# Performance work log

Measured on AMD Instinct MI355X. Metric: run time of the kernel, lower is better.

## Reference

```python
import jax, jax.numpy as jnp
import numpy as np

B, T, C = 2, 1024, 2048
HEAD_SIZE = 64
H = C // HEAD_SIZE          # 32 heads
N_LAYER, LAYER_ID = 24, 12
D_MIX_LORA = 32
LN_EPS = 1e-5


def _layer_norm(x, g, b):
    mu = jnp.mean(x, axis=-1, keepdims=True)
    var = jnp.mean(jnp.square(x - mu), axis=-1, keepdims=True)
    return (x - mu) * jax.lax.rsqrt(var + LN_EPS) * g + b


def setup_inputs() -> dict:
    key = jax.random.key(0)
    ks = jax.random.split(key, 8)
    # data-dependent init of time_maa_* exactly as in the torch module
    r01 = LAYER_ID / (N_LAYER - 1)
    r1a0 = 1.0 - LAYER_ID / N_LAYER
    ddd = np.arange(C, dtype=np.float32) / C
    time_maa_x = jnp.asarray(1.0 - np.power(ddd, r1a0), dtype=jnp.float32)
    time_maa_r = jnp.asarray(1.0 - np.power(ddd, 0.5 * r1a0), dtype=jnp.float32)
    time_maa_k = jnp.asarray(1.0 - np.power(ddd, r1a0), dtype=jnp.float32)
    time_maa_v = jnp.asarray(1.0 - (np.power(ddd, r1a0) + 0.3 * r01), dtype=jnp.float32)
    # LoRA mix weights (w1 is zero-init in the module, keep small random for a nontrivial test)
    w1 = jax.random.uniform(ks[0], (C, D_MIX_LORA * 3), jnp.float32, -0.01, 0.01)
    w2 = jax.random.uniform(ks[1], (3, D_MIX_LORA, C), jnp.float32, -0.01, 0.01)
    scale = 1.0 / np.sqrt(C)
    Wq = jax.random.normal(ks[2], (C, C), jnp.float32) * scale  # stored as [in, out]
    Wk = jax.random.normal(ks[3], (C, C), jnp.float32) * scale
    Wv = jax.random.normal(ks[4], (C, C), jnp.float32) * scale
    Wo = jax.random.normal(ks[5], (C, C), jnp.float32) * scale
    ones = jnp.ones((C,), jnp.float32)
    zeros = jnp.zeros((C,), jnp.float32)
    # rotary angles, standard half-dim frequencies over head_size
    Kd = HEAD_SIZE
    inv_freq = 1.0 / (10000.0 ** (np.arange(0, Kd, 2, dtype=np.float32) / Kd))
    ang = np.outer(np.arange(T, dtype=np.float32), inv_freq)  # [T, Kd//2]
    cos = jnp.asarray(np.cos(ang), jnp.float32)
    sin = jnp.asarray(np.sin(ang), jnp.float32)
    x = jax.random.normal(ks[6], (B, T, C), jnp.float32)
    shift_state = jax.random.normal(ks[7], (B, C), jnp.float32)
    return {
        "x": x, "shift_state": shift_state,
        "time_maa_x": time_maa_x, "time_maa_r": time_maa_r,
        "time_maa_k": time_maa_k, "time_maa_v": time_maa_v,
        "w1": w1, "w2": w2,
        "Wq": Wq, "Wk": Wk, "Wv": Wv, "Wo": Wo,
        "g_r": ones, "b_r": zeros, "g_k": ones, "b_k": zeros,
        "g_v": ones, "b_v": zeros, "g_x": ones, "b_x": zeros,
        "cos": cos, "sin": sin,
    }


def reference(x, shift_state, time_maa_x, time_maa_r, time_maa_k, time_maa_v,
              w1, w2, Wq, Wk, Wv, Wo,
              g_r, b_r, g_k, b_k, g_v, b_v, g_x, b_x, cos, sin):
    Bv, Tv, Cv = x.shape
    Kd = Cv // H
    # token shift: prepend previous-step state, diff against current
    xprev = jnp.concatenate([shift_state[:, None, :], x[:, :-1]], axis=1)
    dxprev = xprev - x
    # data-dependent LoRA mixing coefficients
    xxx = x + dxprev * time_maa_x                      # [B,T,C]
    h = jnp.tanh(xxx @ w1).reshape(Bv, Tv, 3, D_MIX_LORA)
    m = jnp.einsum('btli,lic->lbtc', h, w2)            # [3,B,T,C]
    mr, mk, mv = m[0], m[1], m[2]
    xq = x + dxprev * (time_maa_r + mr)
    xk = x + dxprev * (time_maa_k + mk)
    xv = x + dxprev * (time_maa_v + mv)
    q = _layer_norm(xq @ Wq, g_r, b_r)
    k = _layer_norm(xk @ Wk, g_k, b_k)
    v = _layer_norm(xv @ Wv, g_v, b_v)
    # [B,H,T,K]
    q = q.reshape(Bv, Tv, H, Kd).transpose(0, 2, 1, 3)
    k = k.reshape(Bv, Tv, H, Kd).transpose(0, 2, 1, 3)
    v = v.reshape(Bv, Tv, H, Kd).transpose(0, 2, 1, 3)
    # rotary embedding (half split)
    c = cos[None, None, :, :]
    s = sin[None, None, :, :]
    def rope(t):
        t1, t2 = t[..., :Kd // 2], t[..., Kd // 2:]
        return jnp.concatenate([t1 * c - t2 * s, t1 * s + t2 * c], axis=-1)
    q, k = rope(q), rope(k)
    # causal SDPA
    scores = jnp.einsum('bhtd,bhsd->bhts', q, k) / np.sqrt(Kd)
    mask = jnp.tril(jnp.ones((Tv, Tv), dtype=bool))
    scores = jnp.where(mask, scores, jnp.finfo(scores.dtype).min)
    attn = jax.nn.softmax(scores, axis=-1)
    o = jnp.einsum('bhts,bhsd->bhtd', attn, v)
    o = o.transpose(0, 2, 1, 3).reshape(Bv, Tv, Cv)
    o = _layer_norm(o, g_x, b_x)
    return o @ Wo
```

## Files before the change

### kernel.cpp

```cpp
#include <hip/hip_runtime.h>
#include <math.h>

static constexpr int BB = 2;
static constexpr int TT = 1024;
static constexpr int CC = 2048;
static constexpr int HH = 32;
static constexpr int KD = 64;
static constexpr int BT = BB * TT;

typedef short   v8s  __attribute__((ext_vector_type(8)));
typedef float   v4f  __attribute__((ext_vector_type(4)));
typedef unsigned short u16;
typedef u16     u16x8 __attribute__((ext_vector_type(8)));
typedef u16     u16x4 __attribute__((ext_vector_type(4)));
typedef float   fx4  __attribute__((ext_vector_type(4)));

__device__ __forceinline__ u16 f2bf(float f) {
    unsigned u = __builtin_bit_cast(unsigned, f);
    u = u + 0x7FFFu + ((u >> 16) & 1u);
    return (u16)(u >> 16);
}
__device__ __forceinline__ float bf2f(u16 v) {
    return __builtin_bit_cast(float, ((unsigned)v) << 16);
}

__device__ __forceinline__ void gld16(const u16* g, u16* l) {
    __builtin_amdgcn_global_load_lds(
        (const __attribute__((address_space(1))) void*)g,
        (__attribute__((address_space(3))) void*)l, 16, 0, 0);
}

__device__ __forceinline__ void cstore(float* p, float v) { *p = v; }
__device__ __forceinline__ void cstore(u16* p, float v)   { *p = f2bf(v); }

__device__ __forceinline__ void xcd_map(int bid, int& bx, int& by) {
    int i = bid & 7;
    int j = bid >> 3;
    bx = (i & 3) * 4 + (j & 3);
    by = (i >> 2) * 8 + (j >> 2);
}

__global__ __launch_bounds__(256) void k_tconv5(const float* __restrict__ W0,
                                                const float* __restrict__ W1,
                                                const float* __restrict__ W2,
                                                const float* __restrict__ W3,
                                                const float* __restrict__ w1,
                                                u16* __restrict__ T0, u16* __restrict__ T1,
                                                u16* __restrict__ T2, u16* __restrict__ T3,
                                                u16* __restrict__ w1t) {
    __shared__ float tile[64][97];
    int tid = threadIdx.x;
    int z = blockIdx.z;
    if (z == 4) {
        if (blockIdx.y != 0) return;
        int kb = blockIdx.x * 64;
        for (int i = tid; i < 64 * 96; i += 256) {
            int r = i / 96, c = i - r * 96;
            tile[r][c] = w1[(size_t)(kb + r) * 96 + c];
        }
        __syncthreads();
        for (int i = tid; i < 96 * 64; i += 256) {
            int n = i >> 6, k = i & 63;
            w1t[(size_t)n * CC + kb + k] = f2bf(tile[k][n]);
        }
        return;
    }
    const float* W = (z == 0) ? W0 : (z == 1) ? W1 : (z == 2) ? W2 : W3;
    u16* Wt = (z == 0) ? T0 : (z == 1) ? T1 : (z == 2) ? T2 : T3;
    int nb = blockIdx.x * 64, kb = blockIdx.y * 64;
    for (int i = tid; i < 4096; i += 256) {
        int r = i >> 6, c = i & 63;
        tile[r][c] = W[(size_t)(kb + r) * CC + nb + c];
    }
    __syncthreads();
    for (int i = tid; i < 4096; i += 256) {
        int r = i >> 6, c = i & 63;
        Wt[(size_t)(nb + r) * CC + kb + c] = f2bf(tile[c][r]);
    }
}

__global__ __launch_bounds__(128) void k_lgemm(const float* __restrict__ x,
                                               const float* __restrict__ shift,
                                               const float* __restrict__ maa_x,
                                               const u16* __restrict__ w1t,
                                               float* __restrict__ hp) {
    __shared__ u16 As[16 * 64];
    __shared__ u16 Bs[96 * 64];
    int tid = threadIdx.x, lane = tid & 63, wave = tid >> 6;
    int brow = blockIdx.x * 16;
    int kbeg = blockIdx.y * 512;

    int ar = tid >> 3, ag = tid & 7;
    int grow = brow + ar;
    int t = grow & (TT - 1), b = grow >> 10;
    const float* xr = x + (size_t)grow * CC;
    const float* xp = (t == 0) ? (shift + (size_t)b * CC) : (xr - CC);
    u16* adst = As + ar * 64 + ((ag ^ (ar & 7)) * 8);

    v4f acc[3];
    #pragma unroll
    for (int ni = 0; ni < 3; ++ni)
        #pragma unroll
        for (int e = 0; e < 4; ++e) acc[ni][e] = 0.f;

    for (int k0 = kbeg; k0 < kbeg + 512; k0 += 64) {
        __syncthreads();
        #pragma unroll
        for (int u = 0; u < 6; ++u) {
            int r = (wave * 6 + u) * 8 + (lane >> 3);
            int sc = ((lane & 7) ^ (r & 7)) * 8;
            gld16(w1t + (size_t)r * CC + k0 + sc, Bs + (wave * 6 + u) * 512);
        }
        {
            int kb_ = k0 + ag * 8;
            fx4 x0 = *reinterpret_cast<const fx4*>(xr + kb_);
            fx4 x1 = *reinterpret_cast<const fx4*>(xr + kb_ + 4);
            fx4 p0 = *reinterpret_cast<const fx4*>(xp + kb_);
            fx4 p1 = *reinterpret_cast<const fx4*>(xp + kb_ + 4);
            fx4 m0 = *reinterpret_cast<const fx4*>(maa_x + kb_);
            fx4 m1 = *reinterpret_cast<const fx4*>(maa_x + kb_ + 4);
            fx4 r0 = x0 + (p0 - x0) * m0;
            fx4 r1 = x1 + (p1 - x1) * m1;
            u16x8 a8;
            #pragma unroll
            for (int e = 0; e < 4; ++e) { a8[e] = f2bf(r0[e]); a8[e + 4] = f2bf(r1[e]); }
            *reinterpret_cast<u16x8*>(adst) = a8;
        }
        __syncthreads();

        #pragma unroll
        for (int ks = 0; ks < 2; ++ks) {
            int kg = ks * 4 + (lane >> 4);
            int rlA = lane & 15;
            v8s af = *reinterpret_cast<const v8s*>(As + rlA * 64 + ((kg ^ (rlA & 7)) * 8));
            #pragma unroll
            for (int ni = 0; ni < 3; ++ni) {
                int rlB = wave * 48 + ni * 16 + (lane & 15);
                v8s bf = *reinterpret_cast<const v8s*>(Bs + rlB * 64 + ((kg ^ (rlB & 7)) * 8));
                acc[ni] = __builtin_amdgcn_mfma_f32_16x16x32_bf16(af, bf, acc[ni], 0, 0, 0);
            }
        }
    }

    float* hpk = hp + (size_t)blockIdx.y * BT * 96;
    #pragma unroll
    for (int ni = 0; ni < 3; ++ni) {
        int col = wave * 48 + ni * 16 + (lane & 15);
        #pragma unroll
        for (int j = 0; j < 4; ++j) {
            int row = brow + (lane >> 4) * 4 + j;
            hpk[(size_t)row * 96 + col] = acc[ni][j];
        }
    }
}

__global__ __launch_bounds__(256) void k_lred(const float* __restrict__ hp,
                                              float* __restrict__ h) {
    int i = (blockIdx.x * 256 + threadIdx.x) * 4;
    const size_t S = (size_t)BT * 96;
    fx4 a = *reinterpret_cast<const fx4*>(hp + i);
    fx4 b = *reinterpret_cast<const fx4*>(hp + S + i);
    fx4 c = *reinterpret_cast<const fx4*>(hp + 2 * S + i);
    fx4 d = *reinterpret_cast<const fx4*>(hp + 3 * S + i);
    fx4 s = a + b + c + d;
    fx4 o;
    #pragma unroll
    for (int e = 0; e < 4; ++e) o[e] = tanhf(s[e]);
    *reinterpret_cast<fx4*>(h + i) = o;
}

__global__ __launch_bounds__(256) void k_mix2(const float* __restrict__ x,
                                              const float* __restrict__ shift,
                                              const float* __restrict__ h_in,
                                              const float* __restrict__ w2,
                                              const float* __restrict__ maa_r,
                                              const float* __restrict__ maa_k,
                                              const float* __restrict__ maa_v,
                                              u16* __restrict__ oq,
                                              u16* __restrict__ ok,
                                              u16* __restrict__ ov) {
    __shared__ float w2s[96][64];
    __shared__ float hs[64][100];
    int tid = threadIdx.x;
    int c0 = blockIdx.x * 64, r0 = blockIdx.y * 64;
    for (int i = tid; i < 96 * 64; i += 256) {
        int r = i >> 6, c = i & 63;
        w2s[r][c] = w2[(size_t)r * CC + c0 + c];
    }
    for (int i = tid; i < 64 * 96; i += 256) {
        int r = i / 96, jj = i - r * 96;
        hs[r][jj] = h_in[(size_t)(r0 + r) * 96 + jj];
    }
    __syncthreads();

    int cq = tid & 15, rg = tid >> 4;
    int c = c0 + cq * 4;
    fx4 acc[4][3];
    #pragma unroll
    for (int r = 0; r < 4; ++r)
        #pragma unroll
        for (int l = 0; l < 3; ++l)
            #pragma unroll
            for (int e = 0; e < 4; ++e) acc[r][l][e] = 0.f;

    #pragma unroll 2
    for (int i4 = 0; i4 < 8; ++i4) {
        fx4 hv[4][3];
        #pragma unroll
        for (int r = 0; r < 4; ++r) {
            int row = rg * 4 + r;
            hv[r][0] = *reinterpret_cast<const fx4*>(&hs[row][i4 * 4]);
            hv[r][1] = *reinterpret_cast<const fx4*>(&hs[row][32 + i4 * 4]);
            hv[r][2] = *reinterpret_cast<const fx4*>(&hs[row][64 + i4 * 4]);
        }
        #pragma unroll
        for (int e = 0; e < 4; ++e) {
            int i = i4 * 4 + e;
            fx4 w0 = *reinterpret_cast<const fx4*>(&w2s[i][cq * 4]);
            fx4 w1v = *reinterpret_cast<const fx4*>(&w2s[32 + i][cq * 4]);
            fx4 w2v = *reinterpret_cast<const fx4*>(&w2s[64 + i][cq * 4]);
            #pragma unroll
            for (int r = 0; r < 4; ++r) {
                acc[r][0] += hv[r][0][e] * w0;
                acc[r][1] += hv[r][1][e] * w1v;
                acc[r][2] += hv[r][2][e] * w2v;
            }
        }
    }

    fx4 m_r = *reinterpret_cast<const fx4*>(maa_r + c);
    fx4 m_k = *reinterpret_cast<const fx4*>(maa_k + c);
    fx4 m_v = *reinterpret_cast<const fx4*>(maa_v + c);
    #pragma unroll
    for (int r = 0; r < 4; ++r) {
        int grow = r0 + rg * 4 + r;
        int t = grow & (TT - 1), b = grow >> 10;
        const float* xr = x + (size_t)grow * CC;
        const float* xp = (t == 0) ? (shift + (size_t)b * CC) : (xr - CC);
        fx4 xv = *reinterpret_cast<const fx4*>(xr + c);
        fx4 pv = *reinterpret_cast<const fx4*>(xp + c);
        fx4 dx = pv - xv;
        fx4 rq = xv + dx * (m_r + acc[r][0]);
        fx4 rk = xv + dx * (m_k + acc[r][1]);
        fx4 rv = xv + dx * (m_v + acc[r][2]);
        u16x4 pq, pk, pvv;
        #pragma unroll
        for (int e = 0; e < 4; ++e) { pq[e] = f2bf(rq[e]); pk[e] = f2bf(rk[e]); pvv[e] = f2bf(rv[e]); }
        size_t o = (size_t)grow * CC + c;
        *reinterpret_cast<u16x4*>(oq + o) = pq;
        *reinterpret_cast<u16x4*>(ok + o) = pk;
        *reinterpret_cast<u16x4*>(ov + o) = pvv;
    }
}

template <typename CT>
__device__ __forceinline__ void gemm_body(const u16* __restrict__ A,
                                          const u16* __restrict__ Bt,
                                          CT* __restrict__ C,
                                          int bm, int bn) {
    constexpr int Kd = 2048, Nd = 2048;
    __shared__ u16 As[128 * 64];
    __shared__ u16 Bs[128 * 64];
    int tid = threadIdx.x;
    int lane = tid & 63, wave = tid >> 6;
    int wr = wave >> 1, wc = wave & 1;

    int srow[4], scol[4];
    #pragma unroll
    for (int q = 0; q < 4; ++q) {
        int e = q * 2048 + wave * 512 + lane * 8;
        int row = e >> 6;
        srow[q] = row;
        scol[q] = ((lane & 7) ^ (row & 7)) * 8;
    }

    v4f acc[4][4];
    #pragma unroll
    for (int i = 0; i < 4; ++i)
        #pragma unroll
        for (int j = 0; j < 4; ++j)
            #pragma unroll
            for (int e = 0; e < 4; ++e) acc[i][j][e] = 0.f;

    for (int k0 = 0; k0 < Kd; k0 += 64) {
        __syncthreads();
        #pragma unroll
        for (int q = 0; q < 4; ++q)
            gld16(A + (size_t)(bm + srow[q]) * Kd + k0 + scol[q], As + q * 2048 + wave * 512);
        #pragma unroll
        for (int q = 0; q < 4; ++q)
            gld16(Bt + (size_t)(bn + srow[q]) * Kd + k0 + scol[q], Bs + q * 2048 + wave * 512);
        __syncthreads();
        #pragma unroll
        for (int ks = 0; ks < 2; ++ks) {
            int kg = ks * 4 + (lane >> 4);
            v8s af[4], bf[4];
            #pragma unroll
            for (int mi = 0; mi < 4; ++mi) {
                int rl = wr * 64 + mi * 16 + (lane & 15);
                af[mi] = *reinterpret_cast<const v8s*>(As + rl * 64 + ((kg ^ (rl & 7)) * 8));
            }
            #pragma unroll
            for (int ni = 0; ni < 4; ++ni) {
                int rl = wc * 64 + ni * 16 + (lane & 15);
                bf[ni] = *reinterpret_cast<const v8s*>(Bs + rl * 64 + ((kg ^ (rl & 7)) * 8));
            }
            #pragma unroll
            for (int mi = 0; mi < 4; ++mi)
                #pragma unroll
                for (int ni = 0; ni < 4; ++ni)
                    acc[mi][ni] = __builtin_amdgcn_mfma_f32_16x16x32_bf16(af[mi], bf[ni], acc[mi][ni], 0, 0, 0);
        }
    }

    int cr = (lane >> 4) * 4;
    int ccol = lane & 15;
    #pragma unroll
    for (int mi = 0; mi < 4; ++mi)
        #pragma unroll
        for (int ni = 0; ni < 4; ++ni) {
            CT* cp = C + (size_t)(bm + wr * 64 + mi * 16 + cr) * Nd + bn + wc * 64 + ni * 16 + ccol;
            #pragma unroll
            for (int j = 0; j < 4; ++j) cstore(cp + (size_t)j * Nd, acc[mi][ni][j]);
        }
}

__global__ __launch_bounds__(256) void k_gemm_qkv(const u16* A0, const u16* A1, const u16* A2,
                                                  const u16* B0, const u16* B1, const u16* B2,
                                                  u16* C0, u16* C1, u16* C2) {
    int z = blockIdx.y;
    const u16* A = (z == 0) ? A0 : (z == 1) ? A1 : A2;
    const u16* B = (z == 0) ? B0 : (z == 1) ? B1 : B2;
    u16* C = (z == 0) ? C0 : (z == 1) ? C1 : C2;
    int bx, by;
    xcd_map(blockIdx.x, bx, by);
    gemm_body<u16>(A, B, C, by * 128, bx * 128);
}

__global__ __launch_bounds__(256) void k_gemm1(const u16* __restrict__ A,
                                               const u16* __restrict__ Bt,
                                               float* __restrict__ C) {
    int bx, by;
    xcd_map(blockIdx.x, bx, by);
    gemm_body<float>(A, Bt, C, by * 128, bx * 128);
}

__global__ __launch_bounds__(256) void k_ln_bb(u16* __restrict__ y, const u16* __restrict__ xin,
                                               const float* __restrict__ g, const float* __restrict__ bb) {
    int row = blockIdx.x;
    const u16* xr = xin + (size_t)row * CC;
    int tid = threadIdx.x;
    u16x8 v8 = *reinterpret_cast<const u16x8*>(xr + tid * 8);
    float xv[8];
    float s = 0.f, ss = 0.f;
    #pragma unroll
    for (int e = 0; e < 8; ++e) { xv[e] = bf2f(v8[e]); s += xv[e]; ss += xv[e] * xv[e]; }
    #pragma unroll
    for (int o = 32; o > 0; o >>= 1) { s += __shfl_xor(s, o); ss += __shfl_xor(ss, o); }
    __shared__ float red[8];
    int wid = tid >> 6;
    if ((tid & 63) == 0) { red[wid] = s; red[wid + 4] = ss; }
    __syncthreads();
    s  = red[0] + red[1] + red[2] + red[3];
    ss = red[4] + red[5] + red[6] + red[7];
    float mu  = s * (1.0f / CC);
    float var = ss * (1.0f / CC) - mu * mu;
    float rsg = rsqrtf(var + 1e-5f);
    fx4 g0 = *reinterpret_cast<const fx4*>(g + tid * 8);
    fx4 g1 = *reinterpret_cast<const fx4*>(g + tid * 8 + 4);
    fx4 b0 = *reinterpret_cast<const fx4*>(bb + tid * 8);
    fx4 b1 = *reinterpret_cast<const fx4*>(bb + tid * 8 + 4);
    u16x8 o8;
    #pragma unroll
    for (int e = 0; e < 4; ++e) o8[e]     = f2bf((xv[e] - mu) * rsg * g0[e] + b0[e]);
    #pragma unroll
    for (int e = 0; e < 4; ++e) o8[e + 4] = f2bf((xv[e + 4] - mu) * rsg * g1[e] + b1[e]);
    *reinterpret_cast<u16x8*>(y + (size_t)row * CC + tid * 8) = o8;
}

__global__ __launch_bounds__(256) void k_lnrope(const u16* __restrict__ qin,
                                                const u16* __restrict__ kin,
                                                u16* __restrict__ qo, u16* __restrict__ ko,
                                                const float* __restrict__ g_r, const float* __restrict__ b_r,
                                                const float* __restrict__ g_k, const float* __restrict__ b_k,
                                                const float* __restrict__ cosb, const float* __restrict__ sinb) {
    int row = blockIdx.x;
    int t = row & (TT - 1);
    int tid = threadIdx.x;
    const u16* qr_ = qin + (size_t)row * CC;
    const u16* kr_ = kin + (size_t)row * CC;
    float sq = 0.f, ssq = 0.f, sk = 0.f, ssk = 0.f;
    {
        u16x8 qv = *reinterpret_cast<const u16x8*>(qr_ + tid * 8);
        u16x8 kv = *reinterpret_cast<const u16x8*>(kr_ + tid * 8);
        #pragma unroll
        for (int e = 0; e < 8; ++e) {
            float qf = bf2f(qv[e]), kf = bf2f(kv[e]);
            sq += qf; ssq += qf * qf;
            sk += kf; ssk += kf * kf;
        }
    }
    #pragma unroll
    for (int o_ = 32; o_ > 0; o_ >>= 1) {
        sq += __shfl_xor(sq, o_); ssq += __shfl_xor(ssq, o_);
        sk += __shfl_xor(sk, o_); ssk += __shfl_xor(ssk, o_);
    }
    __shared__ float red[16];
    int wid = tid >> 6;
    if ((tid & 63) == 0) { red[wid] = sq; red[wid + 4] = ssq; red[wid + 8] = sk; red[wid + 12] = ssk; }
    __syncthreads();
    sq  = red[0] + red[1] + red[2] + red[3];
    ssq = red[4] + red[5] + red[6] + red[7];
    sk  = red[8] + red[9] + red[10] + red[11];
    ssk = red[12] + red[13] + red[14] + red[15];
    float muq = sq * (1.0f / CC), vq = ssq * (1.0f / CC) - muq * muq, rq = rsqrtf(vq + 1e-5f);
    float muk = sk * (1.0f / CC), vk = ssk * (1.0f / CC) - muk * muk, rk = rsqrtf(vk + 1e-5f);
    #pragma unroll
    for (int i = 0; i < 4; ++i) {
        int p = tid + i * 256;
        int h = p >> 5, d = p & 31;
        int c1 = h * 64 + d, c2 = c1 + 32;
        float cv = cosb[t * 32 + d], sv = sinb[t * 32 + d];
        float q1 = (bf2f(qr_[c1]) - muq) * rq * g_r[c1] + b_r[c1];
        float q2 = (bf2f(qr_[c2]) - muq) * rq * g_r[c2] + b_r[c2];
        qo[(size_t)row * CC + c1] = f2bf((q1 * cv - q2 * sv) * 0.125f);
        qo[(size_t)row * CC + c2] = f2bf((q1 * sv + q2 * cv) * 0.125f);
        float k1 = (bf2f(kr_[c1]) - muk) * rk * g_k[c1] + b_k[c1];
        float k2 = (bf2f(kr_[c2]) - muk) * rk * g_k[c2] + b_k[c2];
        ko[(size_t)row * CC + c1] = f2bf(k1 * cv - k2 * sv);
        ko[(size_t)row * CC + c2] = f2bf(k1 * sv + k2 * cv);
    }
}

__global__ __launch_bounds__(256) void k_vtr(const u16* __restrict__ vin,
                                             u16* __restrict__ vout) {
    int t0 = blockIdx.x * 64, h = blockIdx.y, b = blockIdx.z;
    __shared__ u16 tile[64][72];
    int tid = threadIdx.x;
    #pragma unroll
    for (int u = 0; u < 2; ++u) {
        int g = tid + u * 256;
        int r = g >> 3, gc = g & 7;
        u16x8 vv = *reinterpret_cast<const u16x8*>(vin + (size_t)(b * TT + t0 + r) * CC + h * 64 + gc * 8);
        *reinterpret_cast<u16x8*>(&tile[r][gc * 8]) = vv;
    }
    __syncthreads();
    #pragma unroll
    for (int u = 0; u < 2; ++u) {
        int g = tid + u * 256;
        int d = g >> 3, tc = g & 7;
        u16x8 ov;
        #pragma unroll
        for (int e = 0; e < 8; ++e) ov[e] = tile[tc * 8 + e][d];
        *reinterpret_cast<u16x8*>(vout + ((size_t)(b * HH + h) * KD + d) * TT + t0 + tc * 8) = ov;
    }
}

__global__ __launch_bounds__(512) void k_mattn3(const u16* __restrict__ q,
                                                const u16* __restrict__ k,
                                                const u16* __restrict__ vt,
                                                u16* __restrict__ o) {
    int st = (int)gridDim.x - 1 - (int)blockIdx.x;
    int h = blockIdx.y, b = blockIdx.z;
    __shared__ u16 Ks[2][64 * 64];
    __shared__ u16 Vs[2][64 * 64];
    __shared__ u16 Ps[8][16 * 64];
    int tid = threadIdx.x, lane = tid & 63, wave = tid >> 6;
    size_t bh = (size_t)b * TT * CC + (size_t)h * KD;
    const u16* vth = vt + (size_t)(b * HH + h) * KD * TT;
    int qrow0 = st * 128 + wave * 16;

    v8s qf[2];
    {
        const u16* qp = q + bh + (size_t)(qrow0 + (lane & 15)) * CC + (lane >> 4) * 8;
        qf[0] = *reinterpret_cast<const v8s*>(qp);
        qf[1] = *reinterpret_cast<const v8s*>(qp + 32);
    }

    float mstat[4], lstat[4];
    v4f oacc[4];
    #pragma unroll
    for (int j = 0; j < 4; ++j) { mstat[j] = -1e30f; lstat[j] = 0.f; }
    #pragma unroll
    for (int nd = 0; nd < 4; ++nd)
        #pragma unroll
        for (int e = 0; e < 4; ++e) oacc[nd][e] = 0.f;

    int srow = (wave << 3) + (lane >> 3);
    int scol = ((lane & 7) ^ (srow & 7)) << 3;
    u16* pw = Ps[wave];
    int ktmax = 2 * st + 1;

    auto STAGE = [&](int slot, int kt) {
        gld16(k + bh + (size_t)(kt * 64 + srow) * CC + scol, &Ks[slot][wave * 512]);
        gld16(vth + (size_t)srow * TT + kt * 64 + scol, &Vs[slot][wave * 512]);
    };

    STAGE(0, 0);
    STAGE(1, 1);

    for (int kt = 0; kt <= ktmax; ++kt) {
        int cur = kt & 1;
        if (kt < ktmax) asm volatile("s_waitcnt vmcnt(2)" ::: "memory");
        else            asm volatile("s_waitcnt vmcnt(0)" ::: "memory");
        __builtin_amdgcn_s_barrier();
        __builtin_amdgcn_sched_barrier(0);

        if (kt * 64 <= qrow0 + 15) {
            const u16* KsC = Ks[cur];
            const u16* VsC = Vs[cur];

            v4f s[4];
            __builtin_amdgcn_s_setprio(1);
            #pragma unroll
            for (int ni = 0; ni < 4; ++ni) {
                #pragma unroll
                for (int e = 0; e < 4; ++e) s[ni][e] = 0.f;
                #pragma unroll
                for (int ks = 0; ks < 2; ++ks) {
                    int rl = ni * 16 + (lane & 15);
                    int kg = ks * 4 + (lane >> 4);
                    int swz = kg ^ (rl & 7);
                    v8s kf = *reinterpret_cast<const v8s*>(KsC + rl * 64 + swz * 8);
                    s[ni] = __builtin_amdgcn_mfma_f32_16x16x32_bf16(qf[ks], kf, s[ni], 0, 0, 0);
                }
            }
            __builtin_amdgcn_s_setprio(0);
            if (kt * 64 + 63 > qrow0) {
                int qr = qrow0 + (lane >> 4) * 4;
                int kc = kt * 64 + (lane & 15);
                #pragma unroll
                for (int ni = 0; ni < 4; ++ni)
                    #pragma unroll
                    for (int j = 0; j < 4; ++j)
                        if (kc + ni * 16 > qr + j) s[ni][j] = -1e30f;
            }

            float alpha[4];
            #pragma unroll
            for (int j = 0; j < 4; ++j) {
                float pm = fmaxf(fmaxf(s[0][j], s[1][j]), fmaxf(s[2][j], s[3][j]));
                pm = fmaxf(pm, __shfl_xor(pm, 1));
                pm = fmaxf(pm, __shfl_xor(pm, 2));
                pm = fmaxf(pm, __shfl_xor(pm, 4));
                pm = fmaxf(pm, __shfl_xor(pm, 8));
                float mn = fmaxf(mstat[j], pm);
                alpha[j] = __expf(mstat[j] - mn);
                float rs = 0.f;
                #pragma unroll
                for (int ni = 0; ni < 4; ++ni) {
                    float p = __expf(s[ni][j] - mn);
                    s[ni][j] = p;
                    rs += p;
                }
                rs += __shfl_xor(rs, 1);
                rs += __shfl_xor(rs, 2);
                rs += __shfl_xor(rs, 4);
                rs += __shfl_xor(rs, 8);
                lstat[j] = lstat[j] * alpha[j] + rs;
                mstat[j] = mn;
            }
            #pragma unroll
            for (int nd = 0; nd < 4; ++nd)
                #pragma unroll
                for (int j = 0; j < 4; ++j) oacc[nd][j] *= alpha[j];

            #pragma unroll
            for (int ni = 0; ni < 4; ++ni) {
                int kc = (lane & 15) + ni * 16;
                #pragma unroll
                for (int j = 0; j < 4; ++j) {
                    int qr = (lane >> 4) * 4 + j;
                    int swz = (kc >> 3) ^ (qr & 7) ^ (qr >> 3);
                    pw[qr * 64 + swz * 8 + (kc & 7)] = f2bf(s[ni][j]);
                }
            }

            v8s pf[2];
            #pragma unroll
            for (int ks = 0; ks < 2; ++ks) {
                int prow = lane & 15;
                int kg = ks * 4 + (lane >> 4);
                int swz = kg ^ (prow & 7) ^ (prow >> 3);
                pf[ks] = *reinterpret_cast<const v8s*>(pw + prow * 64 + swz * 8);
            }
            __builtin_amdgcn_s_setprio(1);
            #pragma unroll
            for (int nd = 0; nd < 4; ++nd) {
                #pragma unroll
                for (int ks = 0; ks < 2; ++ks) {
                    int vrow = nd * 16 + (lane & 15);
                    int vg = ks * 4 + (lane >> 4);
                    int vswz = vg ^ (vrow & 7);
                    v8s vf = *reinterpret_cast<const v8s*>(VsC + vrow * 64 + vswz * 8);
                    oacc[nd] = __builtin_amdgcn_mfma_f32_16x16x32_bf16(pf[ks], vf, oacc[nd], 0, 0, 0);
                }
            }
            __builtin_amdgcn_s_setprio(0);
        }

        __builtin_amdgcn_sched_barrier(0);
        __builtin_amdgcn_s_barrier();
        if (kt + 2 <= ktmax) STAGE(cur, kt + 2);
    }

    #pragma unroll
    for (int j = 0; j < 4; ++j) {
        int qrow = qrow0 + (lane >> 4) * 4 + j;
        float inv = 1.0f / lstat[j];
        #pragma unroll
        for (int nd = 0; nd < 4; ++nd)
            o[bh + (size_t)qrow * CC + (lane & 15) + nd * 16] = f2bf(oacc[nd][j] * inv);
    }
}

extern "C" void kernel_launch(void* const* d_in, const int* in_sizes, int n_in,
                              void* d_out, int out_size, void* d_ws, size_t ws_size,
                              hipStream_t stream) {
    const float* x     = (const float*)d_in[0];
    const float* shift = (const float*)d_in[1];
    const float* maa_x = (const float*)d_in[2];
    const float* maa_r = (const float*)d_in[3];
    const float* maa_k = (const float*)d_in[4];
    const float* maa_v = (const float*)d_in[5];
    const float* w1    = (const float*)d_in[6];
    const float* w2    = (const float*)d_in[7];
    const float* Wq    = (const float*)d_in[8];
    const float* Wk    = (const float*)d_in[9];
    const float* Wv    = (const float*)d_in[10];
    const float* Wo    = (const float*)d_in[11];
    const float* g_r   = (const float*)d_in[12];
    const float* b_r   = (const float*)d_in[13];
    const float* g_k   = (const float*)d_in[14];
    const float* b_k   = (const float*)d_in[15];
    const float* g_v   = (const float*)d_in[16];
    const float* b_v   = (const float*)d_in[17];
    const float* g_x   = (const float*)d_in[18];
    const float* b_x   = (const float*)d_in[19];
    const float* cosb  = (const float*)d_in[20];
    const float* sinb  = (const float*)d_in[21];

    char* w = (char*)d_ws;
    const size_t WB = (size_t)BT * CC * 2;
    u16*   wtq  = (u16*)(w + 0 * WB);
    u16*   wtk  = (u16*)(w + 1 * WB);
    u16*   wtv  = (u16*)(w + 2 * WB);
    u16*   xqb  = (u16*)(w + 3 * WB);
    u16*   xkb  = (u16*)(w + 4 * WB);
    u16*   xvb  = (u16*)(w + 5 * WB);
    u16*   qb16 = (u16*)(w + 6 * WB);
    u16*   kb16 = (u16*)(w + 7 * WB);
    u16*   vb16 = (u16*)(w + 8 * WB);
    u16*   vtb  = (u16*)(w + 9 * WB);
    float* hp   = (float*)(w + 10 * WB);
    float* hb   = (float*)(w + 10 * WB + 0x300000);
    u16*   w1t  = (u16*)(w + 10 * WB + 0x400000);
    u16*   wto  = (u16*)(w + 11 * WB);
    u16*   qbb = (u16*)(w + 3 * WB);
    u16*   kbb = (u16*)(w + 4 * WB);
    u16*   vbb = (u16*)(w + 5 * WB);
    u16*   ob  = (u16*)(w + 6 * WB);
    u16*   oln = (u16*)(w + 7 * WB);
    float* out = (float*)d_out;

    k_tconv5<<<dim3(32, 32, 5), 256, 0, stream>>>(Wq, Wk, Wv, Wo, w1,
                                                  wtq, wtk, wtv, wto, w1t);

    k_lgemm<<<dim3(BT / 16, 4), 128, 0, stream>>>(x, shift, maa_x, w1t, hp);
    k_lred<<<BT * 96 / 1024, 256, 0, stream>>>(hp, hb);
    k_mix2<<<dim3(32, 32), 256, 0, stream>>>(x, shift, hb, w2, maa_r, maa_k, maa_v,
                                             xqb, xkb, xvb);

    k_gemm_qkv<<<dim3(256, 3), 256, 0, stream>>>(xqb, xkb, xvb, wtq, wtk, wtv,
                                                 qb16, kb16, vb16);

    k_lnrope<<<BT, 256, 0, stream>>>(qb16, kb16, qbb, kbb, g_r, b_r, g_k, b_k, cosb, sinb);
    k_ln_bb<<<BT, 256, 0, stream>>>(vbb, vb16, g_v, b_v);
    k_vtr<<<dim3(TT / 64, HH, BB), 256, 0, stream>>>(vbb, vtb);

    k_mattn3<<<dim3(TT / 128, HH, BB), 512, 0, stream>>>(qbb, kbb, vtb, ob);

    k_ln_bb<<<BT, 256, 0, stream>>>(oln, ob, g_x, b_x);
    k_gemm1<<<256, 256, 0, stream>>>(oln, wto, out);
}
```

Measured before the change: 231.3 us.

## Split LoRA GEMM K eightfold, fuse V layernorm into lnrope, lazy softmax rescale

The mix-LoRA GEMM now splits the K dimension into 8 chunks of 256 instead of 4 of 512, so it launches more blocks, and the reduction kernel sums 8 partials. The partial buffer offsets move to make room. The V layernorm is folded into the Q/K layernorm+rope kernel, which removes one launch and one pass over the row. In flash attention, the running max is not updated when the new block max exceeds it by at most 8, which skips the alpha exp and the accumulator rescale. That relies on exp headroom in fp32/bf16 P values.

After: 243.0 us. 1.05x slower.

```diff
diff --git a/kernel.cpp b/kernel.cpp
--- a/kernel.cpp
+++ b/kernel.cpp
@@ -88,7 +88,7 @@
     __shared__ u16 Bs[96 * 64];
     int tid = threadIdx.x, lane = tid & 63, wave = tid >> 6;
     int brow = blockIdx.x * 16;
-    int kbeg = blockIdx.y * 512;
+    int kbeg = blockIdx.y * 256;
 
     int ar = tid >> 3, ag = tid & 7;
     int grow = brow + ar;
@@ -103,7 +103,7 @@
         #pragma unroll
         for (int e = 0; e < 4; ++e) acc[ni][e] = 0.f;
 
-    for (int k0 = kbeg; k0 < kbeg + 512; k0 += 64) {
+    for (int k0 = kbeg; k0 < kbeg + 256; k0 += 64) {
         __syncthreads();
         #pragma unroll
         for (int u = 0; u < 6; ++u) {
@@ -158,11 +158,10 @@
                                               float* __restrict__ h) {
     int i = (blockIdx.x * 256 + threadIdx.x) * 4;
     const size_t S = (size_t)BT * 96;
-    fx4 a = *reinterpret_cast<const fx4*>(hp + i);
-    fx4 b = *reinterpret_cast<const fx4*>(hp + S + i);
-    fx4 c = *reinterpret_cast<const fx4*>(hp + 2 * S + i);
-    fx4 d = *reinterpret_cast<const fx4*>(hp + 3 * S + i);
-    fx4 s = a + b + c + d;
+    fx4 s = *reinterpret_cast<const fx4*>(hp + i);
+    #pragma unroll
+    for (int p = 1; p < 8; ++p)
+        s += *reinterpret_cast<const fx4*>(hp + (size_t)p * S + i);
     fx4 o;
     #pragma unroll
     for (int e = 0; e < 4; ++e) o[e] = tanhf(s[e]);
@@ -378,57 +377,87 @@
     *reinterpret_cast<u16x8*>(y + (size_t)row * CC + tid * 8) = o8;
 }
 
-__global__ __launch_bounds__(256) void k_lnrope(const u16* __restrict__ qin,
-                                                const u16* __restrict__ kin,
-                                                u16* __restrict__ qo, u16* __restrict__ ko,
-                                                const float* __restrict__ g_r, const float* __restrict__ b_r,
-                                                const float* __restrict__ g_k, const float* __restrict__ b_k,
-                                                const float* __restrict__ cosb, const float* __restrict__ sinb) {
+__global__ __launch_bounds__(256) void k_lnrope3(const u16* __restrict__ qin,
+                                                 const u16* __restrict__ kin,
+                                                 const u16* __restrict__ vin,
+                                                 u16* __restrict__ qo, u16* __restrict__ ko,
+                                                 u16* __restrict__ vo,
+                                                 const float* __restrict__ g_r, const float* __restrict__ b_r,
+                                                 const float* __restrict__ g_k, const float* __restrict__ b_k,
+                                                 const float* __restrict__ g_v, const float* __restrict__ b_v,
+                                                 const float* __restrict__ cosb, const float* __restrict__ sinb) {
     int row = blockIdx.x;
     int t = row & (TT - 1);
     int tid = threadIdx.x;
     const u16* qr_ = qin + (size_t)row * CC;
     const u16* kr_ = kin + (size_t)row * CC;
-    float sq = 0.f, ssq = 0.f, sk = 0.f, ssk = 0.f;
+    const u16* vr_ = vin + (size_t)row * CC;
+    float sq = 0.f, ssq = 0.f, sk = 0.f, ssk = 0.f, sv = 0.f, ssv = 0.f;
+    float xv[8];
     {
         u16x8 qv = *reinterpret_cast<const u16x8*>(qr_ + tid * 8);
         u16x8 kv = *reinterpret_cast<const u16x8*>(kr_ + tid * 8);
+        u16x8 vv = *reinterpret_cast<const u16x8*>(vr_ + tid * 8);
         #pragma unroll
         for (int e = 0; e < 8; ++e) {
             float qf = bf2f(qv[e]), kf = bf2f(kv[e]);
+            xv[e] = bf2f(vv[e]);
             sq += qf; ssq += qf * qf;
             sk += kf; ssk += kf * kf;
+            sv += xv[e]; ssv += xv[e] * xv[e];
         }
     }
     #pragma unroll
     for (int o_ = 32; o_ > 0; o_ >>= 1) {
         sq += __shfl_xor(sq, o_); ssq += __shfl_xor(ssq, o_);
         sk += __shfl_xor(sk, o_); ssk += __shfl_xor(ssk, o_);
-    }
-    __shared__ float red[16];
+        sv += __shfl_xor(sv, o_); ssv += __shfl_xor(ssv, o_);
+    }
+    __shared__ float red[24];
     int wid = tid >> 6;
-    if ((tid & 63) == 0) { red[wid] = sq; red[wid + 4] = ssq; red[wid + 8] = sk; red[wid + 12] = ssk; }
+    if ((tid & 63) == 0) {
+        red[wid] = sq; red[wid + 4] = ssq;
+        red[wid + 8] = sk; red[wid + 12] = ssk;
+        red[wid + 16] = sv; red[wid + 20] = ssv;
+    }
     __syncthreads();
     sq  = red[0] + red[1] + red[2] + red[3];
     ssq = red[4] + red[5] + red[6] + red[7];
     sk  = red[8] + red[9] + red[10] + red[11];
     ssk = red[12] + red[13] + red[14] + red[15];
+    sv  = red[16] + red[17] + red[18] + red[19];
+    ssv = red[20] + red[21] + red[22] + red[23];
     float muq = sq * (1.0f / CC), vq = ssq * (1.0f / CC) - muq * muq, rq = rsqrtf(vq + 1e-5f);
     float muk = sk * (1.0f / CC), vk = ssk * (1.0f / CC) - muk * muk, rk = rsqrtf(vk + 1e-5f);
+    float muv = sv * (1.0f / CC), vv_ = ssv * (1.0f / CC) - muv * muv, rv = rsqrtf(vv_ + 1e-5f);
+
+    {
+        fx4 g0 = *reinterpret_cast<const fx4*>(g_v + tid * 8);
+        fx4 g1 = *reinterpret_cast<const fx4*>(g_v + tid * 8 + 4);
+        fx4 b0 = *reinterpret_cast<const fx4*>(b_v + tid * 8);
+        fx4 b1 = *reinterpret_cast<const fx4*>(b_v + tid * 8 + 4);
+        u16x8 o8;
+        #pragma unroll
+        for (int e = 0; e < 4; ++e) o8[e]     = f2bf((xv[e] - muv) * rv * g0[e] + b0[e]);
+        #pragma unroll
+        for (int e = 0; e < 4; ++e) o8[e + 4] = f2bf((xv[e + 4] - muv) * rv * g1[e] + b1[e]);
+        *reinterpret_cast<u16x8*>(vo + (size_t)row * CC + tid * 8) = o8;
+    }
+
     #pragma unroll
     for (int i = 0; i < 4; ++i) {
         int p = tid + i * 256;
         int h = p >> 5, d = p & 31;
         int c1 = h * 64 + d, c2 = c1 + 32;
-        float cv = cosb[t * 32 + d], sv = sinb[t * 32 + d];
+        float cv = cosb[t * 32 + d], sv2 = sinb[t * 32 + d];
         float q1 = (bf2f(qr_[c1]) - muq) * rq * g_r[c1] + b_r[c1];
         float q2 = (bf2f(qr_[c2]) - muq) * rq * g_r[c2] + b_r[c2];
-        qo[(size_t)row * CC + c1] = f2bf((q1 * cv - q2 * sv) * 0.125f);
-        qo[(size_t)row * CC + c2] = f2bf((q1 * sv + q2 * cv) * 0.125f);
+        qo[(size_t)row * CC + c1] = f2bf((q1 * cv - q2 * sv2) * 0.125f);
+        qo[(size_t)row * CC + c2] = f2bf((q1 * sv2 + q2 * cv) * 0.125f);
         float k1 = (bf2f(kr_[c1]) - muk) * rk * g_k[c1] + b_k[c1];
         float k2 = (bf2f(kr_[c2]) - muk) * rk * g_k[c2] + b_k[c2];
-        ko[(size_t)row * CC + c1] = f2bf(k1 * cv - k2 * sv);
-        ko[(size_t)row * CC + c2] = f2bf(k1 * sv + k2 * cv);
+        ko[(size_t)row * CC + c1] = f2bf(k1 * cv - k2 * sv2);
+        ko[(size_t)row * CC + c2] = f2bf(k1 * sv2 + k2 * cv);
     }
 }
 
@@ -536,7 +565,8 @@
                         if (kc + ni * 16 > qr + j) s[ni][j] = -1e30f;
             }
 
-            float alpha[4];
+            float pm4[4];
+            int okl = 1;
             #pragma unroll
             for (int j = 0; j < 4; ++j) {
                 float pm = fmaxf(fmaxf(s[0][j], s[1][j]), fmaxf(s[2][j], s[3][j]));
@@ -544,26 +574,50 @@
                 pm = fmaxf(pm, __shfl_xor(pm, 2));
                 pm = fmaxf(pm, __shfl_xor(pm, 4));
                 pm = fmaxf(pm, __shfl_xor(pm, 8));
-                float mn = fmaxf(mstat[j], pm);
-                alpha[j] = __expf(mstat[j] - mn);
-                float rs = 0.f;
-                #pragma unroll
-                for (int ni = 0; ni < 4; ++ni) {
-                    float p = __expf(s[ni][j] - mn);
-                    s[ni][j] = p;
-                    rs += p;
+                pm4[j] = pm;
+                okl &= (pm - mstat[j] <= 8.0f) ? 1 : 0;
+            }
+            if (__all(okl)) {
+                #pragma unroll
+                for (int j = 0; j < 4; ++j) {
+                    float rs = 0.f;
+                    #pragma unroll
+                    for (int ni = 0; ni < 4; ++ni) {
+                        float p = __expf(s[ni][j] - mstat[j]);
+                        s[ni][j] = p;
+                        rs += p;
+                    }
+                    rs += __shfl_xor(rs, 1);
+                    rs += __shfl_xor(rs, 2);
+                    rs += __shfl_xor(rs, 4);
+                    rs += __shfl_xor(rs, 8);
+                    lstat[j] += rs;
                 }
-                rs += __shfl_xor(rs, 1);
-                rs += __shfl_xor(rs, 2);
-                rs += __shfl_xor(rs, 4);
-                rs += __shfl_xor(rs, 8);
-                lstat[j] = lstat[j] * alpha[j] + rs;
-                mstat[j] = mn;
-            }
-            #pragma unroll
-            for (int nd = 0; nd < 4; ++nd)
-                #pragma unroll
-                for (int j = 0; j < 4; ++j) oacc[nd][j] *= alpha[j];
+            } else {
+                float alpha[4];
+                #pragma unroll
+                for (int j = 0; j < 4; ++j) {
+                    float mn = fmaxf(mstat[j], pm4[j]);
+                    alpha[j] = __expf(mstat[j] - mn);
+                    float rs = 0.f;
+                    #pragma unroll
+                    for (int ni = 0; ni < 4; ++ni) {
+                        float p = __expf(s[ni][j] - mn);
+                        s[ni][j] = p;
+                        rs += p;
+                    }
+                    rs += __shfl_xor(rs, 1);
+                    rs += __shfl_xor(rs, 2);
+                    rs += __shfl_xor(rs, 4);
+                    rs += __shfl_xor(rs, 8);
+                    lstat[j] = lstat[j] * alpha[j] + rs;
+                    mstat[j] = mn;
+                }
+                #pragma unroll
+                for (int nd = 0; nd < 4; ++nd)
+                    #pragma unroll
+                    for (int j = 0; j < 4; ++j) oacc[nd][j] *= alpha[j];
+            }
 
             #pragma unroll
             for (int ni = 0; ni < 4; ++ni) {
@@ -653,8 +707,8 @@
     u16*   vb16 = (u16*)(w + 8 * WB);
     u16*   vtb  = (u16*)(w + 9 * WB);
     float* hp   = (float*)(w + 10 * WB);
-    float* hb   = (float*)(w + 10 * WB + 0x300000);
-    u16*   w1t  = (u16*)(w + 10 * WB + 0x400000);
+    float* hb   = (float*)(w + 10 * WB + 0x600000);
+    u16*   w1t  = (u16*)(w + 10 * WB + 0x700000);
     u16*   wto  = (u16*)(w + 11 * WB);
     u16*   qbb = (u16*)(w + 3 * WB);
     u16*   kbb = (u16*)(w + 4 * WB);
@@ -666,7 +720,7 @@
     k_tconv5<<<dim3(32, 32, 5), 256, 0, stream>>>(Wq, Wk, Wv, Wo, w1,
                                                   wtq, wtk, wtv, wto, w1t);
 
-    k_lgemm<<<dim3(BT / 16, 4), 128, 0, stream>>>(x, shift, maa_x, w1t, hp);
+    k_lgemm<<<dim3(BT / 16, 8), 128, 0, stream>>>(x, shift, maa_x, w1t, hp);
     k_lred<<<BT * 96 / 1024, 256, 0, stream>>>(hp, hb);
     k_mix2<<<dim3(32, 32), 256, 0, stream>>>(x, shift, hb, w2, maa_r, maa_k, maa_v,
                                              xqb, xkb, xvb);
@@ -674,8 +728,8 @@
     k_gemm_qkv<<<dim3(256, 3), 256, 0, stream>>>(xqb, xkb, xvb, wtq, wtk, wtv,
                                                  qb16, kb16, vb16);
 
-    k_lnrope<<<BT, 256, 0, stream>>>(qb16, kb16, qbb, kbb, g_r, b_r, g_k, b_k, cosb, sinb);
-    k_ln_bb<<<BT, 256, 0, stream>>>(vbb, vb16, g_v, b_v);
+    k_lnrope3<<<BT, 256, 0, stream>>>(qb16, kb16, vb16, qbb, kbb, vbb,
+                                      g_r, b_r, g_k, b_k, g_v, b_v, cosb, sinb);
     k_vtr<<<dim3(TT / 64, HH, BB), 256, 0, stream>>>(vbb, vtb);
 
     k_mattn3<<<dim3(TT / 128, HH, BB), 512, 0, stream>>>(qbb, kbb, vtb, ob);
```
